# Kernel tuning notes

Hardware: AMD Instinct MI355X
Metric: run time of the kernel (lower is better)

The kernel has to match this reference:

```python
import jax, jax.numpy as jnp
import numpy as np

NUM_USER = 24000
NUM_ITEM = 8000
DIM_E = 64
V_DIM = 2048
T_DIM = 384
TOPK = 10
N_UI_LAYERS = 2
LAMBDA = 0.9
N_INTER = 400000


def _build_sim(x):
    xn = x / jnp.linalg.norm(x, axis=-1, keepdims=True)
    return xn @ xn.T


def _knn_sym(sim, topk):
    # top-k per row -> sparse graph with symmetric (D^-1/2 A D^-1/2) normalization
    n = sim.shape[0]
    val, ind = jax.lax.top_k(sim, topk)            # [n, k]
    row = jnp.repeat(jnp.arange(n), topk)
    w = val.reshape(-1)
    col = ind.reshape(-1)
    deg = jax.ops.segment_sum(w, row, num_segments=n)
    dis = jnp.where(deg > 0, deg ** -0.5, 0.0)     # inf -> 0 as in torch masked_fill
    return col, dis[row] * w * dis[col]


def setup_inputs() -> dict:
    key = jax.random.key(0)
    ks = jax.random.split(key, 12)
    user_emb = jax.random.normal(ks[0], (NUM_USER, DIM_E), jnp.float32) * 0.1
    item_emb = jax.random.normal(ks[1], (NUM_ITEM, DIM_E), jnp.float32) * 0.1
    v_feat = jax.random.normal(ks[2], (NUM_ITEM, V_DIM), jnp.float32)
    t_feat = jax.random.normal(ks[3], (NUM_ITEM, T_DIM), jnp.float32)
    W_v = jax.random.normal(ks[4], (V_DIM, DIM_E), jnp.float32) * (1.0 / np.sqrt(V_DIM))
    b_v = jnp.zeros((DIM_E,), jnp.float32)
    W_t = jax.random.normal(ks[5], (T_DIM, DIM_E), jnp.float32) * (1.0 / np.sqrt(T_DIM))
    b_t = jnp.zeros((DIM_E,), jnp.float32)
    Wq1 = jax.random.normal(ks[6], (DIM_E, DIM_E), jnp.float32) * (1.0 / np.sqrt(DIM_E))
    bq1 = jnp.zeros((DIM_E,), jnp.float32)
    wq2 = jax.random.normal(ks[7], (DIM_E,), jnp.float32) * (1.0 / np.sqrt(DIM_E))
    # bipartite user-item interaction edges, symmetrized (as in __init__)
    u = jax.random.randint(ks[8], (N_INTER,), 0, NUM_USER)
    it = jax.random.randint(ks[9], (N_INTER,), 0, NUM_ITEM) + NUM_USER
    ei = jnp.stack([u, it])
    edge_index = jnp.concatenate([ei, ei[::-1]], axis=1)  # [2, 2*N_INTER]
    # original (frozen) multimodal KNN graphs built from raw features at init
    orig_img_cols, orig_img_w = _knn_sym(_build_sim(v_feat), TOPK)
    orig_txt_cols, orig_txt_w = _knn_sym(_build_sim(t_feat), TOPK)
    return {"user_emb": user_emb, "item_emb": item_emb, "v_feat": v_feat,
            "t_feat": t_feat, "W_v": W_v, "b_v": b_v, "W_t": W_t, "b_t": b_t,
            "Wq1": Wq1, "bq1": bq1, "wq2": wq2,
            "orig_img_w": orig_img_w, "orig_txt_w": orig_txt_w,
            "edge_index": edge_index,
            "orig_img_cols": orig_img_cols, "orig_txt_cols": orig_txt_cols}


def reference(user_emb, item_emb, v_feat, t_feat, W_v, b_v, W_t, b_t,
              Wq1, bq1, wq2, orig_img_w, orig_txt_w,
              edge_index, orig_img_cols, orig_txt_cols):
    n_user, n_item = user_emb.shape[0], item_emb.shape[0]
    # modality projections
    image_feats = v_feat @ W_v + b_v
    text_feats = t_feat @ W_t + b_t
    # fresh KNN graphs from projected features (build_item_graph=True path)
    img_cols, img_w = _knn_sym(_build_sim(image_feats), TOPK)
    txt_cols, txt_w = _knn_sym(_build_sim(text_feats), TOPK)
    row = jnp.repeat(jnp.arange(n_item), TOPK)

    def fused_spmm(cols_new, w_new, cols_orig, w_orig, x):
        # (1-lam)*A_new + lam*A_orig, applied as a single sparse matmul
        rows = jnp.concatenate([row, row])
        cols = jnp.concatenate([cols_new, cols_orig])
        w = jnp.concatenate([(1.0 - LAMBDA) * w_new,
                             LAMBDA * jax.lax.stop_gradient(w_orig)])
        return jax.ops.segment_sum(w[:, None] * x[cols], rows, num_segments=n_item)

    # NOTE: source bug reproduced - mm_layers loop always re-reads item_embedding,
    # so effective propagation depth is 1 regardless of mm_layers.
    image_item = fused_spmm(img_cols, img_w, orig_img_cols, orig_img_w, item_emb)
    text_item = fused_spmm(txt_cols, txt_w, orig_txt_cols, orig_txt_w, item_emb)

    def q(x):
        return jnp.tanh(x @ Wq1 + bq1) @ wq2  # [n_item]

    att = jnp.stack([q(image_item), q(text_item)], axis=-1)  # [n_item, 2]
    wgt = jax.nn.softmax(att, axis=-1)
    h = wgt[:, :1] * image_item + wgt[:, 1:] * text_item

    # user-item GCN propagation with sym degree normalization
    ego = jnp.concatenate([user_emb, item_emb], axis=0)
    n = ego.shape[0]
    r, c = edge_index[0], edge_index[1]
    deg = jax.ops.segment_sum(jnp.ones_like(r, dtype=ego.dtype), r, num_segments=n)
    dis = jnp.where(deg > 0, deg ** -0.5, 0.0)
    norm = dis[r] * dis[c]
    embs = [ego]
    for _ in range(N_UI_LAYERS):
        ego = jax.ops.segment_sum(norm[:, None] * ego[c], r, num_segments=n)
        embs.append(ego)
    all_emb = jnp.mean(jnp.stack(embs, axis=1), axis=1)
    u_g, i_g = all_emb[:n_user], all_emb[n_user:]
    h_norm = h / jnp.maximum(jnp.linalg.norm(h, axis=1, keepdims=True), 1e-12)
    i_g = i_g + h_norm
    return jnp.concatenate([u_g, i_g], axis=0)
```

## Files before the change

kernel.cpp:

```cpp
#include <hip/hip_runtime.h>
#include <math.h>

#define N_USER 24000
#define N_ITEM 8000
#define N_NODE 32000
#define N_EDGE 800000
#define NJC    10
#define JCH    800
#define NEG_INF -1e30f

typedef __attribute__((ext_vector_type(8))) short bf16x8;
typedef __attribute__((ext_vector_type(4))) float f32x4;

__device__ __forceinline__ float wred_sum(float v) {
#pragma unroll
  for (int off = 32; off; off >>= 1) v += __shfl_xor(v, off, 64);
  return v;
}

__device__ __forceinline__ unsigned short f2bf(float f) {
  unsigned int u = __float_as_uint(f);
  unsigned int r = (u + 0x7fffu + ((u >> 16) & 1u)) >> 16;
  return (unsigned short)r;
}
__device__ __forceinline__ float bf2f(unsigned short h) {
  return __uint_as_float(((unsigned int)h) << 16);
}

__device__ __forceinline__ unsigned int umx(unsigned int a, unsigned int b) { return a > b ? a : b; }
__device__ __forceinline__ unsigned int umn(unsigned int a, unsigned int b) { return a < b ? a : b; }

__device__ __forceinline__ float key_val(unsigned int k) {
  return ((float)(int)(k >> 13) - 131080.0f) * (1.0f / 131072.0f);
}
__device__ __forceinline__ int key_idx(unsigned int k) {
  return 8191 - (int)(k & 8191u);
}

__global__ __launch_bounds__(256) void gemm64(
    const float* __restrict__ X, const float* __restrict__ W,
    float* __restrict__ P, int K, int Klen)
{
  __shared__ float As[32 * 64];
  __shared__ float Bs[32 * 64];
  const int tid = threadIdx.x;
  const int m0 = blockIdx.x * 64;
  const int kc0 = blockIdx.y * Klen;
  float* out = P + (size_t)blockIdx.y * N_ITEM * 64;
  const int tr = tid >> 4, tc = tid & 15;
  float acc[4][4] = {};
  for (int k0 = kc0; k0 < kc0 + Klen; k0 += 32) {
    __syncthreads();
#pragma unroll
    for (int l = 0; l < 2; ++l) {
      int f4 = tid + l * 256;
      int r = f4 >> 3, kq = f4 & 7;
      float4 a = *(const float4*)(X + (size_t)(m0 + r) * K + k0 + kq * 4);
      As[(kq * 4 + 0) * 64 + r] = a.x;
      As[(kq * 4 + 1) * 64 + r] = a.y;
      As[(kq * 4 + 2) * 64 + r] = a.z;
      As[(kq * 4 + 3) * 64 + r] = a.w;
      int kb = f4 >> 4, nq = f4 & 15;
      *(float4*)(Bs + kb * 64 + nq * 4) =
          *(const float4*)(W + (size_t)(k0 + kb) * 64 + nq * 4);
    }
    __syncthreads();
#pragma unroll
    for (int k = 0; k < 32; ++k) {
      float4 a4 = *(const float4*)(As + k * 64 + tr * 4);
      float4 b4 = *(const float4*)(Bs + k * 64 + tc * 4);
      float av[4] = {a4.x, a4.y, a4.z, a4.w};
      float bv[4] = {b4.x, b4.y, b4.z, b4.w};
#pragma unroll
      for (int ri = 0; ri < 4; ++ri)
#pragma unroll
        for (int ci = 0; ci < 4; ++ci) acc[ri][ci] += av[ri] * bv[ci];
    }
  }
#pragma unroll
  for (int ri = 0; ri < 4; ++ri) {
    float4 o;
    o.x = acc[ri][0]; o.y = acc[ri][1]; o.z = acc[ri][2]; o.w = acc[ri][3];
    *(float4*)(out + (size_t)(m0 + tr * 4 + ri) * 64 + tc * 4) = o;
  }
}

__global__ __launch_bounds__(256) void norm_split(
    const float* __restrict__ P, const float* __restrict__ bias,
    unsigned short* __restrict__ Xh, unsigned short* __restrict__ Xl, int nk)
{
  int row = blockIdx.x * 4 + (threadIdx.x >> 6);
  int lane = threadIdx.x & 63;
  size_t o = (size_t)row * 64 + lane;
  float v = bias[lane];
  for (int q = 0; q < nk; ++q) v += P[(size_t)q * N_ITEM * 64 + o];
  float ss = wred_sum(v * v);
  float xn = v * rsqrtf(ss);
  unsigned short hi = f2bf(xn);
  Xh[o] = hi;
  Xl[o] = f2bf(xn - bf2f(hi));
}

__global__ __launch_bounds__(128) void sim_topk_mfma(
    const unsigned short* __restrict__ Xh, const unsigned short* __restrict__ Xl,
    unsigned int* __restrict__ pk)
{
  __shared__ char lds[2 * 2 * 32 * 128];
  const int tid = threadIdx.x;
  const int l = tid & 63;
  const int wid = tid >> 6;
  const int ib = blockIdx.x * 64 + wid * 32;
  const int jc = blockIdx.y * JCH;

  bf16x8 bh[2][2], bl[2][2];
#pragma unroll
  for (int s = 0; s < 2; ++s) {
    int irow = ib + s * 16 + (l & 15);
    int ksl = (l >> 4) * 8;
#pragma unroll
    for (int kh = 0; kh < 2; ++kh) {
      bh[s][kh] = *(const bf16x8*)(Xh + (size_t)irow * 64 + kh * 32 + ksl);
      bl[s][kh] = *(const bf16x8*)(Xl + (size_t)irow * 64 + kh * 32 + ksl);
    }
  }

  unsigned int K0[10], K1[10];
#pragma unroll
  for (int t = 0; t < 10; ++t) { K0[t] = 0u; K1[t] = 0u; }

  auto stage = [&](int b, int p) {
#pragma unroll
    for (int s2 = 0; s2 < 2; ++s2) {
      int u = tid + s2 * 128;
      int row = u >> 3, cb = (u & 7) * 16;
      int gr = jc + p * 32 + row;
      int4 vh = *(const int4*)(Xh + (size_t)gr * 64 + (cb >> 1));
      int4 vl = *(const int4*)(Xl + (size_t)gr * 64 + (cb >> 1));
      int bo = (row * 128 + cb) ^ ((row & 7) << 4);
      *(int4*)(lds + b * 8192 + bo) = vh;
      *(int4*)(lds + b * 8192 + 4096 + bo) = vl;
    }
  };

  stage(0, 0);
  int cur = 0;
  for (int p = 0; p < 25; ++p) {
    __syncthreads();
    if (p < 24) stage(cur ^ 1, p + 1);
    const char* ldsH = lds + cur * 8192;
    const char* ldsL = ldsH + 4096;
    f32x4 acc[2][2] = {};
#pragma unroll
    for (int t = 0; t < 2; ++t) {
      int jr = t * 16 + (l & 15);
      int sw = (jr & 7) << 4;
      int rb = jr * 128 + ((l >> 4) << 4);
      bf16x8 ah0 = *(const bf16x8*)(ldsH + (rb ^ sw));
      bf16x8 ah1 = *(const bf16x8*)(ldsH + ((rb + 64) ^ sw));
      bf16x8 al0 = *(const bf16x8*)(ldsL + (rb ^ sw));
      bf16x8 al1 = *(const bf16x8*)(ldsL + ((rb + 64) ^ sw));
#pragma unroll
      for (int s = 0; s < 2; ++s) {
        acc[t][s] = __builtin_amdgcn_mfma_f32_16x16x32_bf16(ah0, bh[s][0], acc[t][s], 0, 0, 0);
        acc[t][s] = __builtin_amdgcn_mfma_f32_16x16x32_bf16(ah1, bh[s][1], acc[t][s], 0, 0, 0);
        acc[t][s] = __builtin_amdgcn_mfma_f32_16x16x32_bf16(ah0, bl[s][0], acc[t][s], 0, 0, 0);
        acc[t][s] = __builtin_amdgcn_mfma_f32_16x16x32_bf16(ah1, bl[s][1], acc[t][s], 0, 0, 0);
        acc[t][s] = __builtin_amdgcn_mfma_f32_16x16x32_bf16(al0, bh[s][0], acc[t][s], 0, 0, 0);
        acc[t][s] = __builtin_amdgcn_mfma_f32_16x16x32_bf16(al1, bh[s][1], acc[t][s], 0, 0, 0);
      }
    }
    const int jg0 = jc + p * 32 + ((l >> 4) << 2);
#pragma unroll
    for (int s = 0; s < 2; ++s) {
      unsigned int* K = s ? K1 : K0;
#pragma unroll
      for (int t = 0; t < 2; ++t) {
#pragma unroll
        for (int r = 0; r < 4; ++r) {
          float f = acc[t][s][r];
          unsigned int v19 = (unsigned int)(int)(f * 131072.0f + 131080.0f);
          unsigned int key = (v19 << 13) | (unsigned int)(8191 - (jg0 + t * 16 + r));
#pragma unroll
          for (int q = 0; q < 10; ++q) {
            unsigned int mn = umn(K[q], key);
            K[q] = umx(K[q], key);
            key = mn;
          }
        }
      }
    }
    cur ^= 1;
  }

#pragma unroll
  for (int s = 0; s < 2; ++s) {
    unsigned int* K = s ? K1 : K0;
    unsigned int kv[10];
#pragma unroll
    for (int t = 0; t < 10; ++t) {
      unsigned int m = K[0];
      m = umx(m, (unsigned int)__shfl_xor((int)m, 16, 64));
      m = umx(m, (unsigned int)__shfl_xor((int)m, 32, 64));
      bool own = (K[0] == m);
#pragma unroll
      for (int q2 = 0; q2 < 9; ++q2) K[q2] = own ? K[q2 + 1] : K[q2];
      K[9] = own ? 0u : K[9];
      kv[t] = m;
    }
    int i = ib + s * 16 + (l & 15);
    if (l < 16) {
      size_t base = ((size_t)i * NJC + blockIdx.y) * 10;
#pragma unroll
      for (int t = 0; t < 10; ++t) pk[base + t] = kv[t];
    }
  }
}

__global__ __launch_bounds__(256) void merge_topk(
    const unsigned int* __restrict__ pk,
    float* __restrict__ tv, int* __restrict__ tc, float* __restrict__ dis)
{
  int lane = threadIdx.x & 63;
  int row = blockIdx.x * 4 + (threadIdx.x >> 6);
  size_t base = (size_t)row * (NJC * 10);
  unsigned int k0 = pk[base + lane];
  unsigned int k1 = (lane < 36) ? pk[base + 64 + lane] : 0u;
  float deg = 0.f, keepv = 0.f; int keepc = 0;
  for (int t = 0; t < 10; ++t) {
    unsigned int m = umx(k0, k1);
#pragma unroll
    for (int off = 32; off; off >>= 1)
      m = umx(m, (unsigned int)__shfl_xor((int)m, off, 64));
    deg += key_val(m);
    if (k0 == m) k0 = 0u;
    else if (k1 == m) k1 = 0u;
    if (lane == t) { keepv = key_val(m); keepc = key_idx(m); }
  }
  if (lane < 10) { tv[(size_t)row * 10 + lane] = keepv; tc[(size_t)row * 10 + lane] = keepc; }
  if (lane == 0) dis[row] = deg > 0.f ? rsqrtf(deg) : 0.f;
}

__global__ __launch_bounds__(256) void spmm_attn(
    const float* __restrict__ tv_i, const int* __restrict__ tc_i, const float* __restrict__ dis_i,
    const float* __restrict__ ow_i, const int* __restrict__ oc_i,
    const float* __restrict__ tv_t, const int* __restrict__ tc_t, const float* __restrict__ dis_t,
    const float* __restrict__ ow_t, const int* __restrict__ oc_t,
    const float* __restrict__ item_emb,
    const float* __restrict__ Wq1, const float* __restrict__ bq1,
    const float* __restrict__ wq2, float* __restrict__ hn)
{
  __shared__ float Wlds[64 * 64];
  __shared__ float sm[4][2][64];
  int tid = threadIdx.x;
  int lane = tid & 63, wid = tid >> 6;
  int row = blockIdx.x * 4 + wid;
#pragma unroll
  for (int s = 0; s < 4; ++s) {
    int idx = tid + s * 256;
    ((float4*)Wlds)[idx] = ((const float4*)Wq1)[idx];
  }
  float a0 = 0.f, a1 = 0.f;
  {
    float disr = dis_i[row];
#pragma unroll
    for (int t = 0; t < 10; ++t) {
      int c = tc_i[(size_t)row * 10 + t];
      a0 += 0.1f * disr * tv_i[(size_t)row * 10 + t] * dis_i[c] * item_emb[(size_t)c * 64 + lane];
    }
#pragma unroll
    for (int t = 0; t < 10; ++t) {
      int c = oc_i[(size_t)row * 10 + t];
      a0 += 0.9f * ow_i[(size_t)row * 10 + t] * item_emb[(size_t)c * 64 + lane];
    }
  }
  {
    float disr = dis_t[row];
#pragma unroll
    for (int t = 0; t < 10; ++t) {
      int c = tc_t[(size_t)row * 10 + t];
      a1 += 0.1f * disr * tv_t[(size_t)row * 10 + t] * dis_t[c] * item_emb[(size_t)c * 64 + lane];
    }
#pragma unroll
    for (int t = 0; t < 10; ++t) {
      int c = oc_t[(size_t)row * 10 + t];
      a1 += 0.9f * ow_t[(size_t)row * 10 + t] * item_emb[(size_t)c * 64 + lane];
    }
  }
  sm[wid][0][lane] = a0;
  sm[wid][1][lane] = a1;
  __syncthreads();
  float y0 = bq1[lane], y1 = bq1[lane];
  for (int k = 0; k < 64; ++k) {
    float w = Wlds[k * 64 + lane];
    y0 += sm[wid][0][k] * w;
    y1 += sm[wid][1][k] * w;
  }
  float wq = wq2[lane];
  float s0 = wred_sum(tanhf(y0) * wq);
  float s1 = wred_sum(tanhf(y1) * wq);
  float mx = fmaxf(s0, s1);
  float e0 = expf(s0 - mx), e1 = expf(s1 - mx);
  float inv = 1.f / (e0 + e1);
  float h = (e0 * inv) * a0 + (e1 * inv) * a1;
  float n2 = wred_sum(h * h);
  float nrm = fmaxf(sqrtf(n2), 1e-12f);
  hn[(size_t)row * 64 + lane] = h / nrm;
}

__global__ void ui_zero(int* degi, int* cursor)
{
  int n = blockIdx.x * 256 + threadIdx.x;
  if (n < N_NODE) { degi[n] = 0; cursor[n] = 0; }
}

__global__ void ui_count(const int* __restrict__ r, int* degi)
{
  int e = blockIdx.x * 256 + threadIdx.x;
  if (e < N_EDGE) atomicAdd(&degi[r[e]], 1);
}

__global__ __launch_bounds__(256) void ui_blocksum(const int* __restrict__ degi, int* __restrict__ bsum)
{
  __shared__ int ws4[4];
  int tid = threadIdx.x;
  int v = degi[blockIdx.x * 256 + tid];
#pragma unroll
  for (int off = 32; off; off >>= 1) v += __shfl_xor(v, off, 64);
  if ((tid & 63) == 0) ws4[tid >> 6] = v;
  __syncthreads();
  if (tid == 0) bsum[blockIdx.x] = ws4[0] + ws4[1] + ws4[2] + ws4[3];
}

__global__ __launch_bounds__(128) void ui_scanb(const int* __restrict__ bsum, int* __restrict__ bbase, int* __restrict__ offs)
{
  __shared__ int s[128];
  int t = threadIdx.x;
  int v = (t < 125) ? bsum[t] : 0;
  s[t] = v;
  __syncthreads();
  for (int off = 1; off < 128; off <<= 1) {
    int tmp = (t >= off) ? s[t - off] : 0;
    __syncthreads();
    s[t] += tmp;
    __syncthreads();
  }
  if (t < 125) bbase[t] = s[t] - v;
  if (t == 127) offs[N_NODE] = s[127];
}

__global__ __launch_bounds__(256) void ui_scanc(const int* __restrict__ degi, const int* __restrict__ bbase,
                                                int* __restrict__ offs, float* __restrict__ disui)
{
  __shared__ int wt[4];
  int tid = threadIdx.x;
  int i = blockIdx.x * 256 + tid;
  int d = degi[i];
  int v = d;
#pragma unroll
  for (int off = 1; off < 64; off <<= 1) {
    int n = __shfl_up(v, off, 64);
    if ((tid & 63) >= off) v += n;
  }
  if ((tid & 63) == 63) wt[tid >> 6] = v;
  __syncthreads();
  int add = bbase[blockIdx.x];
  for (int w = 0; w < (tid >> 6); ++w) add += wt[w];
  offs[i] = add + v - d;
  disui[i] = d > 0 ? rsqrtf((float)d) : 0.f;
}

__global__ void ui_fill(const int* __restrict__ r, const int* __restrict__ c,
                        const int* __restrict__ offs, int* cursor, int* __restrict__ csr)
{
  int e = blockIdx.x * 256 + threadIdx.x;
  if (e < N_EDGE) {
    int rr = r[e];
    int pos = offs[rr] + atomicAdd(&cursor[rr], 1);
    csr[pos] = c[e];
  }
}

template <bool FIRST, bool FINAL>
__global__ __launch_bounds__(256) void ui_prop(
    const float* __restrict__ in, const float* __restrict__ ue,
    const float* __restrict__ ie, float* __restrict__ out,
    const int* __restrict__ offs, const int* __restrict__ csr,
    const float* __restrict__ dis, const float* __restrict__ hn)
{
  int tid = threadIdx.x;
  int lane = tid & 63, wid = tid >> 6;
  int row = blockIdx.x * 4 + wid;
  int q = lane >> 4, c4 = lane & 15;
  float4 acc = make_float4(0.f, 0.f, 0.f, 0.f);
  int e0 = offs[row], e1 = offs[row + 1];
  for (int e = e0 + q; e < e1; e += 4) {
    int cc = csr[e];
    const float* src = FIRST
        ? (cc < N_USER ? ue + (size_t)cc * 64 : ie + (size_t)(cc - N_USER) * 64)
        : in + (size_t)cc * 64;
    float4 v = *(const float4*)(src + c4 * 4);
    float d = dis[cc];
    acc.x += d * v.x; acc.y += d * v.y; acc.z += d * v.z; acc.w += d * v.w;
  }
#pragma unroll
  for (int off = 16; off <= 32; off <<= 1) {
    acc.x += __shfl_xor(acc.x, off, 64);
    acc.y += __shfl_xor(acc.y, off, 64);
    acc.z += __shfl_xor(acc.z, off, 64);
    acc.w += __shfl_xor(acc.w, off, 64);
  }
  if (q == 0) {
    float dr = dis[row];
    acc.x *= dr; acc.y *= dr; acc.z *= dr; acc.w *= dr;
    if (!FINAL) {
      *(float4*)(out + (size_t)row * 64 + c4 * 4) = acc;
    } else {
      float4 ego = (row < N_USER)
          ? *(const float4*)(ue + (size_t)row * 64 + c4 * 4)
          : *(const float4*)(ie + (size_t)(row - N_USER) * 64 + c4 * 4);
      float4 l1 = *(const float4*)(in + (size_t)row * 64 + c4 * 4);
      float4 o;
      o.x = (ego.x + l1.x + acc.x) * (1.f / 3.f);
      o.y = (ego.y + l1.y + acc.y) * (1.f / 3.f);
      o.z = (ego.z + l1.z + acc.z) * (1.f / 3.f);
      o.w = (ego.w + l1.w + acc.w) * (1.f / 3.f);
      if (row >= N_USER) {
        float4 h = *(const float4*)(hn + (size_t)(row - N_USER) * 64 + c4 * 4);
        o.x += h.x; o.y += h.y; o.z += h.z; o.w += h.w;
      }
      *(float4*)(out + (size_t)row * 64 + c4 * 4) = o;
    }
  }
}

extern "C" void kernel_launch(void* const* d_in, const int* in_sizes, int n_in,
                              void* d_out, int out_size, void* d_ws, size_t ws_size,
                              hipStream_t stream)
{
  (void)in_sizes; (void)n_in; (void)out_size; (void)ws_size;
  const float* user_emb = (const float*)d_in[0];
  const float* item_emb = (const float*)d_in[1];
  const float* v_feat   = (const float*)d_in[2];
  const float* t_feat   = (const float*)d_in[3];
  const float* W_v      = (const float*)d_in[4];
  const float* b_v      = (const float*)d_in[5];
  const float* W_t      = (const float*)d_in[6];
  const float* b_t      = (const float*)d_in[7];
  const float* Wq1      = (const float*)d_in[8];
  const float* bq1      = (const float*)d_in[9];
  const float* wq2      = (const float*)d_in[10];
  const float* ow_i     = (const float*)d_in[11];
  const float* ow_t     = (const float*)d_in[12];
  const int*   eidx     = (const int*)d_in[13];
  const int*   oc_i     = (const int*)d_in[14];
  const int*   oc_t     = (const int*)d_in[15];
  float* out = (float*)d_out;

  char* wp = (char*)d_ws;
  auto alloc = [&](size_t bytes) -> void* {
    void* p = (void*)wp;
    wp += (bytes + 255) & ~(size_t)255;
    return p;
  };
  unsigned int* BIG0 = (unsigned int*)alloc((size_t)N_NODE * 64 * 4 + 1024);
  float*        BIG1 = (float*)alloc((size_t)N_NODE * 64 * 4 + 1024);
  unsigned int* pk = BIG0;
  float* E1 = BIG1;

  float*          Pp  = (float*)alloc((size_t)4 * N_ITEM * 64 * 4);
  unsigned short* Xh  = (unsigned short*)alloc((size_t)N_ITEM * 64 * 2);
  unsigned short* Xl  = (unsigned short*)alloc((size_t)N_ITEM * 64 * 2);
  float* tv_i  = (float*)alloc((size_t)N_ITEM * 10 * 4);
  int*   tc_i  = (int*)  alloc((size_t)N_ITEM * 10 * 4);
  float* dis_i = (float*)alloc((size_t)N_ITEM * 4);
  float* tv_t  = (float*)alloc((size_t)N_ITEM * 10 * 4);
  int*   tc_t  = (int*)  alloc((size_t)N_ITEM * 10 * 4);
  float* dis_t = (float*)alloc((size_t)N_ITEM * 4);
  float* hn    = (float*)alloc((size_t)N_ITEM * 64 * 4);
  int*   degi  = (int*)  alloc((size_t)N_NODE * 4);
  int*   curs  = (int*)  alloc((size_t)N_NODE * 4);
  int*   offs  = (int*)  alloc((size_t)(N_NODE + 1) * 4);
  float* disui = (float*)alloc((size_t)N_NODE * 4);
  int*   csr   = (int*)  alloc((size_t)N_EDGE * 4);
  int*   bsum  = (int*)  alloc((size_t)128 * 4);
  int*   bbase = (int*)  alloc((size_t)128 * 4);

  gemm64<<<dim3(125, 4), 256, 0, stream>>>(v_feat, W_v, Pp, 2048, 512);
  norm_split<<<2000, 256, 0, stream>>>(Pp, b_v, Xh, Xl, 4);
  sim_topk_mfma<<<dim3(125, NJC), 128, 0, stream>>>(Xh, Xl, pk);
  merge_topk<<<2000, 256, 0, stream>>>(pk, tv_i, tc_i, dis_i);
  gemm64<<<dim3(125, 2), 256, 0, stream>>>(t_feat, W_t, Pp, 384, 192);
  norm_split<<<2000, 256, 0, stream>>>(Pp, b_t, Xh, Xl, 2);
  sim_topk_mfma<<<dim3(125, NJC), 128, 0, stream>>>(Xh, Xl, pk);
  merge_topk<<<2000, 256, 0, stream>>>(pk, tv_t, tc_t, dis_t);
  spmm_attn<<<2000, 256, 0, stream>>>(tv_i, tc_i, dis_i, ow_i, oc_i,
                                      tv_t, tc_t, dis_t, ow_t, oc_t,
                                      item_emb, Wq1, bq1, wq2, hn);
  ui_zero<<<125, 256, 0, stream>>>(degi, curs);
  ui_count<<<N_EDGE / 256, 256, 0, stream>>>(eidx, degi);
  ui_blocksum<<<125, 256, 0, stream>>>(degi, bsum);
  ui_scanb<<<1, 128, 0, stream>>>(bsum, bbase, offs);
  ui_scanc<<<125, 256, 0, stream>>>(degi, bbase, offs, disui);
  ui_fill<<<N_EDGE / 256, 256, 0, stream>>>(eidx, eidx + N_EDGE, offs, curs, csr);
  ui_prop<true, false><<<8000, 256, 0, stream>>>(nullptr, user_emb, item_emb, E1, offs, csr, disui, nullptr);
  ui_prop<false, true><<<8000, 256, 0, stream>>>(E1, user_emb, item_emb, out, offs, csr, disui, hn);
}
```

Before: 361.1 us.

## Batch image and text modality kernels into single launches with wider grids

Merges the image and text GEMM, normalize/split, similarity top-k and merge kernels into dual-modality launches using grid y/z dimensions, halving launch count and letting both modalities run concurrently. The K-split for the image GEMM grows to 8 chunks and the text to 3, the sim top-k uses 256-thread blocks covering 128 rows with 16 column chunks of 512, adding bounds clamps for the padded tail. The merge now reduces 160 candidates per row. Workspace is re-laid out so partials and pk share a larger region; more partial traffic and tail handling are the costs.

```diff
diff --git a/kernel.cpp b/kernel.cpp
--- a/kernel.cpp
+++ b/kernel.cpp
@@ -5,9 +5,8 @@
 #define N_ITEM 8000
 #define N_NODE 32000
 #define N_EDGE 800000
-#define NJC    10
-#define JCH    800
-#define NEG_INF -1e30f
+#define NJC    16
+#define JCH    512
 
 typedef __attribute__((ext_vector_type(8))) short bf16x8;
 typedef __attribute__((ext_vector_type(4))) float f32x4;
@@ -37,16 +36,21 @@
   return 8191 - (int)(k & 8191u);
 }
 
-__global__ __launch_bounds__(256) void gemm64(
-    const float* __restrict__ X, const float* __restrict__ W,
-    float* __restrict__ P, int K, int Klen)
+__global__ __launch_bounds__(256) void gemm_dual(
+    const float* __restrict__ Xi, const float* __restrict__ Wi,
+    const float* __restrict__ Xt, const float* __restrict__ Wt,
+    float* __restrict__ Pi, float* __restrict__ Pt)
 {
   __shared__ float As[32 * 64];
   __shared__ float Bs[32 * 64];
   const int tid = threadIdx.x;
   const int m0 = blockIdx.x * 64;
-  const int kc0 = blockIdx.y * Klen;
-  float* out = P + (size_t)blockIdx.y * N_ITEM * 64;
+  const int cy = blockIdx.y;
+  const float* X; const float* W; float* out; int K, kc0, Klen;
+  if (cy < 8) { X = Xi; W = Wi; K = 2048; Klen = 256; kc0 = cy * 256;
+                out = Pi + (size_t)cy * N_ITEM * 64; }
+  else        { X = Xt; W = Wt; K = 384;  Klen = 128; kc0 = (cy - 8) * 128;
+                out = Pt + (size_t)(cy - 8) * N_ITEM * 64; }
   const int tr = tid >> 4, tc = tid & 15;
   float acc[4][4] = {};
   for (int k0 = kc0; k0 < kc0 + Klen; k0 += 32) {
@@ -85,10 +89,15 @@
   }
 }
 
-__global__ __launch_bounds__(256) void norm_split(
-    const float* __restrict__ P, const float* __restrict__ bias,
-    unsigned short* __restrict__ Xh, unsigned short* __restrict__ Xl, int nk)
-{
+__global__ __launch_bounds__(256) void norm_dual(
+    const float* __restrict__ Pi, const float* __restrict__ bi,
+    unsigned short* __restrict__ Xhi, unsigned short* __restrict__ Xli,
+    const float* __restrict__ Pt, const float* __restrict__ bt,
+    unsigned short* __restrict__ Xht, unsigned short* __restrict__ Xlt)
+{
+  const float* P; const float* bias; unsigned short *Xh, *Xl; int nk;
+  if (blockIdx.y == 0) { P = Pi; bias = bi; Xh = Xhi; Xl = Xli; nk = 8; }
+  else                 { P = Pt; bias = bt; Xh = Xht; Xl = Xlt; nk = 3; }
   int row = blockIdx.x * 4 + (threadIdx.x >> 6);
   int lane = threadIdx.x & 63;
   size_t o = (size_t)row * 64 + lane;
@@ -101,21 +110,27 @@
   Xl[o] = f2bf(xn - bf2f(hi));
 }
 
-__global__ __launch_bounds__(128) void sim_topk_mfma(
-    const unsigned short* __restrict__ Xh, const unsigned short* __restrict__ Xl,
+__global__ __launch_bounds__(256) void sim_topk_mfma(
+    const unsigned short* __restrict__ Xhi, const unsigned short* __restrict__ Xli,
+    const unsigned short* __restrict__ Xht, const unsigned short* __restrict__ Xlt,
     unsigned int* __restrict__ pk)
 {
   __shared__ char lds[2 * 2 * 32 * 128];
+  const unsigned short* Xh = blockIdx.z ? Xht : Xhi;
+  const unsigned short* Xl = blockIdx.z ? Xlt : Xli;
+  unsigned int* pkm = pk + (size_t)blockIdx.z * N_ITEM * (NJC * 10);
+
   const int tid = threadIdx.x;
   const int l = tid & 63;
   const int wid = tid >> 6;
-  const int ib = blockIdx.x * 64 + wid * 32;
+  const int ib = blockIdx.x * 128 + wid * 32;
   const int jc = blockIdx.y * JCH;
 
   bf16x8 bh[2][2], bl[2][2];
 #pragma unroll
   for (int s = 0; s < 2; ++s) {
     int irow = ib + s * 16 + (l & 15);
+    if (irow > N_ITEM - 1) irow = N_ITEM - 1;
     int ksl = (l >> 4) * 8;
 #pragma unroll
     for (int kh = 0; kh < 2; ++kh) {
@@ -129,24 +144,21 @@
   for (int t = 0; t < 10; ++t) { K0[t] = 0u; K1[t] = 0u; }
 
   auto stage = [&](int b, int p) {
-#pragma unroll
-    for (int s2 = 0; s2 < 2; ++s2) {
-      int u = tid + s2 * 128;
-      int row = u >> 3, cb = (u & 7) * 16;
-      int gr = jc + p * 32 + row;
-      int4 vh = *(const int4*)(Xh + (size_t)gr * 64 + (cb >> 1));
-      int4 vl = *(const int4*)(Xl + (size_t)gr * 64 + (cb >> 1));
-      int bo = (row * 128 + cb) ^ ((row & 7) << 4);
-      *(int4*)(lds + b * 8192 + bo) = vh;
-      *(int4*)(lds + b * 8192 + 4096 + bo) = vl;
-    }
+    int row = tid >> 3, cb = (tid & 7) * 16;
+    int gr = jc + p * 32 + row;
+    if (gr > N_ITEM - 1) gr = N_ITEM - 1;
+    int4 vh = *(const int4*)(Xh + (size_t)gr * 64 + (cb >> 1));
+    int4 vl = *(const int4*)(Xl + (size_t)gr * 64 + (cb >> 1));
+    int bo = (row * 128 + cb) ^ ((row & 7) << 4);
+    *(int4*)(lds + b * 8192 + bo) = vh;
+    *(int4*)(lds + b * 8192 + 4096 + bo) = vl;
   };
 
   stage(0, 0);
   int cur = 0;
-  for (int p = 0; p < 25; ++p) {
+  for (int p = 0; p < 16; ++p) {
     __syncthreads();
-    if (p < 24) stage(cur ^ 1, p + 1);
+    if (p < 15) stage(cur ^ 1, p + 1);
     const char* ldsH = lds + cur * 8192;
     const char* ldsL = ldsH + 4096;
     f32x4 acc[2][2] = {};
@@ -177,9 +189,11 @@
       for (int t = 0; t < 2; ++t) {
 #pragma unroll
         for (int r = 0; r < 4; ++r) {
+          int jj = jg0 + t * 16 + r;
           float f = acc[t][s][r];
           unsigned int v19 = (unsigned int)(int)(f * 131072.0f + 131080.0f);
-          unsigned int key = (v19 << 13) | (unsigned int)(8191 - (jg0 + t * 16 + r));
+          unsigned int key = (v19 << 13) | (unsigned int)(8191 - jj);
+          key = (jj < N_ITEM) ? key : 0u;
 #pragma unroll
           for (int q = 0; q < 10; ++q) {
             unsigned int mn = umn(K[q], key);
@@ -208,32 +222,38 @@
       kv[t] = m;
     }
     int i = ib + s * 16 + (l & 15);
-    if (l < 16) {
+    if (l < 16 && i < N_ITEM) {
       size_t base = ((size_t)i * NJC + blockIdx.y) * 10;
 #pragma unroll
-      for (int t = 0; t < 10; ++t) pk[base + t] = kv[t];
+      for (int t = 0; t < 10; ++t) pkm[base + t] = kv[t];
     }
   }
 }
 
 __global__ __launch_bounds__(256) void merge_topk(
     const unsigned int* __restrict__ pk,
-    float* __restrict__ tv, int* __restrict__ tc, float* __restrict__ dis)
-{
+    float* __restrict__ tv_i, int* __restrict__ tc_i, float* __restrict__ dis_i,
+    float* __restrict__ tv_t, int* __restrict__ tc_t, float* __restrict__ dis_t)
+{
+  float* tv; int* tc; float* dis;
+  if (blockIdx.y == 0) { tv = tv_i; tc = tc_i; dis = dis_i; }
+  else                 { tv = tv_t; tc = tc_t; dis = dis_t; }
   int lane = threadIdx.x & 63;
   int row = blockIdx.x * 4 + (threadIdx.x >> 6);
-  size_t base = (size_t)row * (NJC * 10);
+  size_t base = (size_t)blockIdx.y * N_ITEM * (NJC * 10) + (size_t)row * (NJC * 10);
   unsigned int k0 = pk[base + lane];
-  unsigned int k1 = (lane < 36) ? pk[base + 64 + lane] : 0u;
+  unsigned int k1 = pk[base + 64 + lane];
+  unsigned int k2 = (lane < 32) ? pk[base + 128 + lane] : 0u;
   float deg = 0.f, keepv = 0.f; int keepc = 0;
   for (int t = 0; t < 10; ++t) {
-    unsigned int m = umx(k0, k1);
+    unsigned int m = umx(umx(k0, k1), k2);
 #pragma unroll
     for (int off = 32; off; off >>= 1)
       m = umx(m, (unsigned int)__shfl_xor((int)m, off, 64));
     deg += key_val(m);
     if (k0 == m) k0 = 0u;
     else if (k1 == m) k1 = 0u;
+    else if (k2 == m) k2 = 0u;
     if (lane == t) { keepv = key_val(m); keepc = key_idx(m); }
   }
   if (lane < 10) { tv[(size_t)row * 10 + lane] = keepv; tc[(size_t)row * 10 + lane] = keepc; }
@@ -462,14 +482,17 @@
     wp += (bytes + 255) & ~(size_t)255;
     return p;
   };
-  unsigned int* BIG0 = (unsigned int*)alloc((size_t)N_NODE * 64 * 4 + 1024);
-  float*        BIG1 = (float*)alloc((size_t)N_NODE * 64 * 4 + 1024);
-  unsigned int* pk = BIG0;
-  float* E1 = BIG1;
-
-  float*          Pp  = (float*)alloc((size_t)4 * N_ITEM * 64 * 4);
-  unsigned short* Xh  = (unsigned short*)alloc((size_t)N_ITEM * 64 * 2);
-  unsigned short* Xl  = (unsigned short*)alloc((size_t)N_ITEM * 64 * 2);
+  char* regionA = (char*)alloc((size_t)8 * N_ITEM * 64 * 4 + 1024);
+  char* regionB = (char*)alloc((size_t)N_NODE * 64 * 4 + 1024);
+  float* Pp_i = (float*)regionA;
+  float* Pp_t = (float*)regionB;
+  unsigned int* pk = (unsigned int*)regionA;
+  float* E1 = (float*)regionB;
+
+  unsigned short* Xhi = (unsigned short*)alloc((size_t)N_ITEM * 64 * 2);
+  unsigned short* Xli = (unsigned short*)alloc((size_t)N_ITEM * 64 * 2);
+  unsigned short* Xht = (unsigned short*)alloc((size_t)N_ITEM * 64 * 2);
+  unsigned short* Xlt = (unsigned short*)alloc((size_t)N_ITEM * 64 * 2);
   float* tv_i  = (float*)alloc((size_t)N_ITEM * 10 * 4);
   int*   tc_i  = (int*)  alloc((size_t)N_ITEM * 10 * 4);
   float* dis_i = (float*)alloc((size_t)N_ITEM * 4);
@@ -485,14 +508,10 @@
   int*   bsum  = (int*)  alloc((size_t)128 * 4);
   int*   bbase = (int*)  alloc((size_t)128 * 4);
 
-  gemm64<<<dim3(125, 4), 256, 0, stream>>>(v_feat, W_v, Pp, 2048, 512);
-  norm_split<<<2000, 256, 0, stream>>>(Pp, b_v, Xh, Xl, 4);
-  sim_topk_mfma<<<dim3(125, NJC), 128, 0, stream>>>(Xh, Xl, pk);
-  merge_topk<<<2000, 256, 0, stream>>>(pk, tv_i, tc_i, dis_i);
-  gemm64<<<dim3(125, 2), 256, 0, stream>>>(t_feat, W_t, Pp, 384, 192);
-  norm_split<<<2000, 256, 0, stream>>>(Pp, b_t, Xh, Xl, 2);
-  sim_topk_mfma<<<dim3(125, NJC), 128, 0, stream>>>(Xh, Xl, pk);
-  merge_topk<<<2000, 256, 0, stream>>>(pk, tv_t, tc_t, dis_t);
+  gemm_dual<<<dim3(125, 11), 256, 0, stream>>>(v_feat, W_v, t_feat, W_t, Pp_i, Pp_t);
+  norm_dual<<<dim3(2000, 2), 256, 0, stream>>>(Pp_i, b_v, Xhi, Xli, Pp_t, b_t, Xht, Xlt);
+  sim_topk_mfma<<<dim3(63, NJC, 2), 256, 0, stream>>>(Xhi, Xli, Xht, Xlt, pk);
+  merge_topk<<<dim3(2000, 2), 256, 0, stream>>>(pk, tv_i, tc_i, dis_i, tv_t, tc_t, dis_t);
   spmm_attn<<<2000, 256, 0, stream>>>(tv_i, tc_i, dis_i, ow_i, oc_i,
                                       tv_t, tc_t, dis_t, ow_t, oc_t,
                                       item_emb, Wq1, bq1, wq2, hn);
```

Result: faster. 320.0 us (-11.4%).
